# Kernel optimization log

Hardware: AMD Instinct MI355X
Metric: run time of the kernel (lower is better)

## Reference

```python
import jax, jax.numpy as jnp
import numpy as np

NUM_EXPERTS = 8
TOP_K = 2
EMBED = 1024
FFN = 2048
GATE_HID = 1024


def setup_inputs() -> dict:
    key = jax.random.key(0)
    ks = jax.random.split(key, 8)
    s_e = 1.0 / np.sqrt(EMBED)
    s_f = 1.0 / np.sqrt(FFN)
    s_g = 1.0 / np.sqrt(GATE_HID)
    return {
        "hidden_states": jax.random.normal(ks[0], (2, 2048, EMBED), dtype=jnp.float32),
        # gate: Linear(EMBED->GATE_HID) with bias, ELU, Linear(GATE_HID->NUM_EXPERTS) with bias
        "gw1": jax.random.uniform(ks[1], (EMBED, GATE_HID), jnp.float32, -s_e, s_e),
        "gb1": jax.random.uniform(ks[2], (GATE_HID,), jnp.float32, -s_e, s_e),
        "gw2": jax.random.uniform(ks[3], (GATE_HID, NUM_EXPERTS), jnp.float32, -s_g, s_g),
        "gb2": jax.random.uniform(ks[4], (NUM_EXPERTS,), jnp.float32, -s_g, s_g),
        # experts (bias=False): w1,w3: EMBED->FFN ; w2: FFN->EMBED, stacked over experts
        "w1": jax.random.uniform(ks[5], (NUM_EXPERTS, EMBED, FFN), jnp.float32, -s_e, s_e),
        "w3": jax.random.uniform(ks[6], (NUM_EXPERTS, EMBED, FFN), jnp.float32, -s_e, s_e),
        "w2": jax.random.uniform(ks[7], (NUM_EXPERTS, FFN, EMBED), jnp.float32, -s_f, s_f),
    }


def reference(hidden_states, gw1, gb1, gw2, gb2, w1, w3, w2):
    B, S, H = hidden_states.shape
    x = hidden_states.reshape(-1, H)                      # [T, H]
    T = x.shape[0]
    # gate MLP
    g = jax.nn.elu(x @ gw1 + gb1)
    router_logits = g @ gw2 + gb2                         # [T, E]
    probs = jax.nn.softmax(router_logits.astype(jnp.float32), axis=-1)
    rw, sel = jax.lax.top_k(probs, TOP_K)                 # [T, K]
    rw = rw / jnp.sum(rw, axis=-1, keepdims=True)
    rw = rw.astype(hidden_states.dtype)
    # combine weights per (token, expert); full-capacity MoE == weighted sum
    combine = jnp.zeros((T, NUM_EXPERTS), dtype=hidden_states.dtype)
    combine = combine.at[jnp.arange(T)[:, None], sel].add(rw)   # [T, E]
    # expert MLPs computed densely then combined (math identical to gather/scatter)
    h = jax.nn.relu(jnp.einsum('th,ehf->etf', x, w1)) * jnp.einsum('th,ehf->etf', x, w3)
    y = jnp.einsum('etf,efh->eth', h, w2)                 # [E, T, H]
    out = jnp.einsum('eth,te->th', y, combine)            # [T, H]
    return out.reshape(B, S, H), router_logits
```

## Files before the change

kernel.cpp:

```cpp
#include <hip/hip_runtime.h>
#include <hip/hip_bf16.h>
#include <stdint.h>

#define TOKENS 4096
#define HDIM   1024
#define FDIM   2048
#define NEXP   8
#define NSLOTS (2 * TOKENS)
#define SLOTPAD (NSLOTS + 128)
#define RISKY_CAP 256
#define FLAG_THR 6e-3f

typedef __attribute__((ext_vector_type(4))) float        f32x4v;
typedef __attribute__((ext_vector_type(2))) float        f32x2v;
typedef __attribute__((ext_vector_type(4))) unsigned int u32x4v;
typedef __attribute__((ext_vector_type(8))) _Float16     f16x8v;

__device__ __forceinline__ unsigned short f2h(float f) {
  _Float16 h = (_Float16)f;
  union { _Float16 h; unsigned short u; } x; x.h = h; return x.u;
}

__device__ __forceinline__ void gload16(void* lds, const void* g) {
  __builtin_amdgcn_global_load_lds(
      reinterpret_cast<const __attribute__((address_space(1))) uint32_t*>(
          reinterpret_cast<uintptr_t>(g)),
      reinterpret_cast<__attribute__((address_space(3))) uint32_t*>(
          reinterpret_cast<uintptr_t>(lds)),
      16, 0, 0);
}

__global__ void k_convert_xh(const float* __restrict__ in, unsigned short* __restrict__ out) {
  const int i = (blockIdx.x * 256 + threadIdx.x) * 8;
  f32x4v a = *(const f32x4v*)(in + i);
  f32x4v b = *(const f32x4v*)(in + i + 4);
  u32x4v r;
  r[0] = (uint32_t)f2h(a[0]) | ((uint32_t)f2h(a[1]) << 16);
  r[1] = (uint32_t)f2h(a[2]) | ((uint32_t)f2h(a[3]) << 16);
  r[2] = (uint32_t)f2h(b[0]) | ((uint32_t)f2h(b[1]) << 16);
  r[3] = (uint32_t)f2h(b[2]) | ((uint32_t)f2h(b[3]) << 16);
  *(u32x4v*)(out + i) = r;
}

__device__ __forceinline__ void transpose_tile_v2(const float* __restrict__ ip,
                                                  unsigned short* __restrict__ op,
                                                  int R, int C, int r0, int c0) {
  __shared__ unsigned short tile[64][70];
  const int t = threadIdx.x;
  const int cp = (t & 15) * 4;
  const int rp = (t >> 4) * 2;
#pragma unroll
  for (int p = 0; p < 2; ++p) {
    const int r = rp + p * 32;
    f32x4v v0 = *(const f32x4v*)(ip + (size_t)(r0 + r) * C + c0 + cp);
    f32x4v v1 = *(const f32x4v*)(ip + (size_t)(r0 + r + 1) * C + c0 + cp);
#pragma unroll
    for (int j = 0; j < 4; ++j)
      *(uint32_t*)&tile[cp + j][r] = (uint32_t)f2h(v0[j]) | ((uint32_t)f2h(v1[j]) << 16);
  }
  __syncthreads();
  const int c = t >> 2, rc = (t & 3) * 16;
  uint32_t q[8];
#pragma unroll
  for (int j = 0; j < 8; ++j) q[j] = *(uint32_t*)&tile[c][rc + j * 2];
  unsigned short* o = op + (size_t)(c0 + c) * R + r0 + rc;
  u32x4v s0, s1;
  s0[0] = q[0]; s0[1] = q[1]; s0[2] = q[2]; s0[3] = q[3];
  s1[0] = q[4]; s1[1] = q[5]; s1[2] = q[6]; s1[3] = q[7];
  *(u32x4v*)o = s0;
  *(u32x4v*)(o + 8) = s1;
}

__global__ __launch_bounds__(256)
void k_transpose_v2(const float* __restrict__ in, unsigned short* __restrict__ out,
                    int R, int C) {
  const size_t mat = (size_t)R * C;
  transpose_tile_v2(in + (size_t)blockIdx.z * mat, out + (size_t)blockIdx.z * mat,
                    R, C, blockIdx.y * 64, blockIdx.x * 64);
}

__global__ __launch_bounds__(256)
void k_transpose_w13_v2(const float* __restrict__ w1, const float* __restrict__ w3,
                        unsigned short* __restrict__ o1, unsigned short* __restrict__ o3) {
  const int R = 1024, C = 2048;
  const size_t mat = (size_t)R * C;
  const int e = blockIdx.z & 7, which = blockIdx.z >> 3;
  const float* ip = (which ? w3 : w1) + (size_t)e * mat;
  unsigned short* op = (which ? o3 : o1) + (size_t)e * mat;
  transpose_tile_v2(ip, op, R, C, blockIdx.y * 64, blockIdx.x * 64);
}

__global__ __launch_bounds__(256)
void k_gate_f16(const unsigned short* __restrict__ Xh, const unsigned short* __restrict__ Bt,
                const float* __restrict__ gb1, float* __restrict__ G) {
  const int n0 = blockIdx.x * 64, m0 = blockIdx.y * 128;
  __shared__ unsigned short lA[128 * 64];
  __shared__ unsigned short lB[64 * 64];
  const int t = threadIdx.x, lane = t & 63, wv = t >> 6;

  const unsigned short *ap[4], *bp[2];
#pragma unroll
  for (int i = 0; i < 4; ++i) {
    const int gi = wv * 4 + i;
    const int row = gi * 8 + (lane >> 3);
    const int cs = (lane & 7) ^ (row & 7);
    ap[i] = Xh + (size_t)(m0 + row) * HDIM + cs * 8;
  }
#pragma unroll
  for (int i = 0; i < 2; ++i) {
    const int gi = wv * 2 + i;
    const int row = gi * 8 + (lane >> 3);
    const int cs = (lane & 7) ^ (row & 7);
    bp[i] = Bt + (size_t)(n0 + row) * HDIM + cs * 8;
  }

  f32x4v acc[4][2];
#pragma unroll
  for (int m = 0; m < 4; ++m)
#pragma unroll
    for (int n = 0; n < 2; ++n) acc[m][n] = (f32x4v){0.f, 0.f, 0.f, 0.f};

  const int wr = (wv >> 1) * 64, wc = (wv & 1) * 32;

  for (int k0 = 0; k0 < HDIM; k0 += 64) {
#pragma unroll
    for (int i = 0; i < 4; ++i) gload16(lA + (wv * 4 + i) * 512, ap[i] + k0);
#pragma unroll
    for (int i = 0; i < 2; ++i) gload16(lB + (wv * 2 + i) * 512, bp[i] + k0);
    __syncthreads();
#pragma unroll
    for (int kk = 0; kk < 2; ++kk) {
      const int ch = kk * 4 + (lane >> 4);
      f16x8v af[4];
#pragma unroll
      for (int m = 0; m < 4; ++m) {
        const int r = wr + m * 16 + (lane & 15);
        af[m] = *(const f16x8v*)(lA + r * 64 + (ch ^ (r & 7)) * 8);
      }
#pragma unroll
      for (int n = 0; n < 2; ++n) {
        const int r = wc + n * 16 + (lane & 15);
        f16x8v b = *(const f16x8v*)(lB + r * 64 + (ch ^ (r & 7)) * 8);
#pragma unroll
        for (int m = 0; m < 4; ++m)
          acc[m][n] = __builtin_amdgcn_mfma_f32_16x16x32_f16(af[m], b, acc[m][n], 0, 0, 0);
      }
    }
    __syncthreads();
  }
#pragma unroll
  for (int m = 0; m < 4; ++m)
#pragma unroll
    for (int n = 0; n < 2; ++n)
#pragma unroll
      for (int q = 0; q < 4; ++q) {
        const int row = m0 + wr + m * 16 + ((lane >> 4) << 2) + q;
        const int col = n0 + wc + n * 16 + (lane & 15);
        float x = acc[m][n][q] + gb1[col];
        G[(size_t)row * 1024 + col] = x > 0.f ? x : expm1f(x);
      }
}

__global__ void k_logits(const float* __restrict__ G, const float* __restrict__ gw2,
                         const float* __restrict__ gb2, float* __restrict__ Lg,
                         int* __restrict__ risky, int* __restrict__ rcnt) {
  const int lane = threadIdx.x & 63, wv = threadIdx.x >> 6;
  const int tok = blockIdx.x * 4 + wv;
  const float* g = G + (size_t)tok * 1024 + lane * 16;
  float acc[8];
#pragma unroll
  for (int j = 0; j < 8; ++j) acc[j] = 0.f;
#pragma unroll
  for (int c = 0; c < 16; c += 4) {
    f32x4v gv = *(const f32x4v*)(g + c);
#pragma unroll
    for (int u = 0; u < 4; ++u) {
      const float* wrow = gw2 + (size_t)(lane * 16 + c + u) * 8;
      f32x4v w0 = *(const f32x4v*)wrow;
      f32x4v w1 = *(const f32x4v*)(wrow + 4);
#pragma unroll
      for (int j = 0; j < 4; ++j) {
        acc[j]     += gv[u] * w0[j];
        acc[j + 4] += gv[u] * w1[j];
      }
    }
  }
#pragma unroll
  for (int s = 1; s < 64; s <<= 1)
#pragma unroll
    for (int j = 0; j < 8; ++j) acc[j] += __shfl_xor(acc[j], s, 64);
  if (lane == 0) {
    float l[8];
#pragma unroll
    for (int j = 0; j < 8; ++j) { l[j] = acc[j] + gb2[j]; Lg[(size_t)tok * 8 + j] = l[j]; }
    int i0 = 0; float v0 = l[0];
#pragma unroll
    for (int j = 1; j < 8; ++j) if (l[j] > v0) { v0 = l[j]; i0 = j; }
    int i1 = (i0 == 0) ? 1 : 0; float v1 = l[i1];
#pragma unroll
    for (int j = 0; j < 8; ++j) if (j != i0 && l[j] > v1) { v1 = l[j]; i1 = j; }
    float v2 = -1e30f;
#pragma unroll
    for (int j = 0; j < 8; ++j) if (j != i0 && j != i1 && l[j] > v2) v2 = l[j];
    if (v1 - v2 < FLAG_THR) {
      const int pos = atomicAdd(rcnt, 1);
      if (pos < RISKY_CAP) risky[pos] = tok;
    }
  }
}

__global__ __launch_bounds__(256)
void k_fixup_gs(const float* __restrict__ X, const float* __restrict__ gw1,
                const float* __restrict__ gb1, const int* __restrict__ risky,
                const int* __restrict__ rcnt, float* __restrict__ gsbuf) {
  __shared__ float xs[1024];
  __shared__ float red[128];
  int n = *rcnt; if (n > RISKY_CAP) n = RISKY_CAP;
  const int idx = blockIdx.y;
  if (idx >= n) return;
  const int tok = risky[idx];
  const int s0 = blockIdx.x * 128;
  const int t = threadIdx.x;
  for (int i = t; i < 1024; i += 256) xs[i] = X[(size_t)tok * 1024 + i];
  __syncthreads();
  const int h = t & 127, kh = t >> 7;
  const float* wp = gw1 + (size_t)(kh * 512) * 1024 + s0 + h;
  const float* xp = xs + kh * 512;
  float a0 = 0.f, a1 = 0.f, a2 = 0.f, a3 = 0.f;
  for (int k = 0; k < 512; k += 4) {
    a0 += xp[k]     * wp[(size_t)k * 1024];
    a1 += xp[k + 1] * wp[(size_t)(k + 1) * 1024];
    a2 += xp[k + 2] * wp[(size_t)(k + 2) * 1024];
    a3 += xp[k + 3] * wp[(size_t)(k + 3) * 1024];
  }
  const float acc = (a0 + a1) + (a2 + a3);
  if (kh == 1) red[h] = acc;
  __syncthreads();
  if (kh == 0) {
    const float v = acc + red[h] + gb1[s0 + h];
    gsbuf[(size_t)idx * 1024 + s0 + h] = v > 0.f ? v : expm1f(v);
  }
}

__global__ __launch_bounds__(256)
void k_fixup_lg(const float* __restrict__ gsbuf, const float* __restrict__ gw2,
                const float* __restrict__ gb2, const int* __restrict__ risky,
                const int* __restrict__ rcnt, float* __restrict__ Lg) {
  __shared__ float part[4][8];
  int n = *rcnt; if (n > RISKY_CAP) n = RISKY_CAP;
  const int idx = blockIdx.x;
  if (idx >= n) return;
  const int tok = risky[idx];
  const int t = threadIdx.x, lane = t & 63, wv = t >> 6;
  float lacc[8];
#pragma unroll
  for (int e = 0; e < 8; ++e) lacc[e] = 0.f;
#pragma unroll
  for (int j = 0; j < 4; ++j) {
    const int k = t * 4 + j;
    const float gv = gsbuf[(size_t)idx * 1024 + k];
    const float* w = gw2 + (size_t)k * 8;
#pragma unroll
    for (int e = 0; e < 8; ++e) lacc[e] += gv * w[e];
  }
#pragma unroll
  for (int s = 1; s < 64; s <<= 1)
#pragma unroll
    for (int e = 0; e < 8; ++e) lacc[e] += __shfl_xor(lacc[e], s, 64);
  if (lane == 0) {
#pragma unroll
    for (int e = 0; e < 8; ++e) part[wv][e] = lacc[e];
  }
  __syncthreads();
  if (t < 8) Lg[(size_t)tok * 8 + t] = part[0][t] + part[1][t] + part[2][t] + part[3][t] + gb2[t];
}

__global__ void k_top2(const float* __restrict__ Lg, int* __restrict__ tok_e,
                       float* __restrict__ tok_w, int* __restrict__ counts) {
  const int t = blockIdx.x * 256 + threadIdx.x;
  float l[8];
#pragma unroll
  for (int j = 0; j < 8; ++j) l[j] = Lg[(size_t)t * 8 + j];
  float mx = l[0];
#pragma unroll
  for (int j = 1; j < 8; ++j) mx = fmaxf(mx, l[j]);
  float p[8];
#pragma unroll
  for (int j = 0; j < 8; ++j) p[j] = expf(l[j] - mx);
  int i0 = 0; float b0 = p[0];
#pragma unroll
  for (int j = 1; j < 8; ++j) if (p[j] > b0) { b0 = p[j]; i0 = j; }
  int i1 = (i0 == 0) ? 1 : 0; float b1 = p[i1];
#pragma unroll
  for (int j = 0; j < 8; ++j) if (j != i0 && p[j] > b1) { b1 = p[j]; i1 = j; }
  const float inv = 1.f / (b0 + b1);
  tok_e[2 * t] = i0; tok_e[2 * t + 1] = i1;
  tok_w[2 * t] = b0 * inv; tok_w[2 * t + 1] = b1 * inv;
  atomicAdd(&counts[i0], 1);
  atomicAdd(&counts[i1], 1);
}

__global__ void k_offsets(const int* __restrict__ counts, int* __restrict__ offs,
                          int* __restrict__ curs) {
  if (threadIdx.x == 0) {
    int a = 0;
#pragma unroll
    for (int e = 0; e < NEXP; ++e) { offs[e] = a; a += counts[e]; }
  }
  if (threadIdx.x < NEXP) curs[threadIdx.x] = 0;
}

__global__ void k_assign(const int* __restrict__ tok_e, const float* __restrict__ tok_w,
                         const int* __restrict__ offs, int* __restrict__ curs,
                         int* __restrict__ slot_tok, float* __restrict__ slot_w,
                         int* __restrict__ tok2slot) {
  const int t = blockIdx.x * 256 + threadIdx.x;
#pragma unroll
  for (int k = 0; k < 2; ++k) {
    const int e = tok_e[2 * t + k];
    const int pos = atomicAdd(&curs[e], 1);
    const int slot = offs[e] + pos;
    slot_tok[slot] = t;
    slot_w[slot] = tok_w[2 * t + k];
    tok2slot[2 * t + k] = slot;
  }
}

__global__ __launch_bounds__(256, 2)
void k_gemm1(const unsigned short* __restrict__ Xh, const unsigned short* __restrict__ w1T,
             const unsigned short* __restrict__ w3T, const int* __restrict__ slot_tok,
             const int* __restrict__ counts, const int* __restrict__ offs,
             unsigned short* __restrict__ Hout) {
  const int e = blockIdx.z;
  const int cnt = counts[e];
  const int mt = blockIdx.y;
  if (mt * 128 >= cnt) return;
  const int base = offs[e] + mt * 128;
  const int n0 = blockIdx.x * 128;

  __shared__ unsigned short lA[128 * 64];
  __shared__ unsigned short lB1[128 * 64];
  __shared__ unsigned short lB3[128 * 64];
  __shared__ int tokid[128];

  const int t = threadIdx.x;
  if (t < 128) tokid[t] = slot_tok[base + t];
  __syncthreads();

  const int lane = t & 63, wv = t >> 6;
  const unsigned short *arow[4], *b1row[4], *b3row[4];
#pragma unroll
  for (int i = 0; i < 4; ++i) {
    const int gi = wv * 4 + i;
    const int row = gi * 8 + (lane >> 3);
    const int cs = (lane & 7) ^ (row & 7);
    arow[i] = Xh + (size_t)tokid[row] * HDIM + cs * 8;
    const int f = n0 + row;
    b1row[i] = w1T + ((size_t)e * FDIM + f) * HDIM + cs * 8;
    b3row[i] = w3T + ((size_t)e * FDIM + f) * HDIM + cs * 8;
  }

  f32x4v acc1[4][4], acc3[4][4];
#pragma unroll
  for (int m = 0; m < 4; ++m)
#pragma unroll
    for (int n = 0; n < 4; ++n) {
      acc1[m][n] = (f32x4v){0.f, 0.f, 0.f, 0.f};
      acc3[m][n] = (f32x4v){0.f, 0.f, 0.f, 0.f};
    }
  const int wr = (wv >> 1) * 64, wc = (wv & 1) * 64;

  for (int k0 = 0; k0 < HDIM; k0 += 64) {
#pragma unroll
    for (int i = 0; i < 4; ++i) {
      gload16(lA + (wv * 4 + i) * 512, arow[i] + k0);
      gload16(lB1 + (wv * 4 + i) * 512, b1row[i] + k0);
      gload16(lB3 + (wv * 4 + i) * 512, b3row[i] + k0);
    }
    __syncthreads();
#pragma unroll
    for (int kk = 0; kk < 64; kk += 32) {
      const int ch = (kk >> 3) + (lane >> 4);
      f16x8v af[4];
#pragma unroll
      for (int m = 0; m < 4; ++m) {
        const int r = wr + m * 16 + (lane & 15);
        af[m] = *(const f16x8v*)(lA + r * 64 + (ch ^ (r & 7)) * 8);
      }
#pragma unroll
      for (int n = 0; n < 4; ++n) {
        const int r = wc + n * 16 + (lane & 15);
        const int o = r * 64 + (ch ^ (r & 7)) * 8;
        f16x8v b1 = *(const f16x8v*)(lB1 + o);
        f16x8v b3 = *(const f16x8v*)(lB3 + o);
#pragma unroll
        for (int m = 0; m < 4; ++m) {
          acc1[m][n] = __builtin_amdgcn_mfma_f32_16x16x32_f16(af[m], b1, acc1[m][n], 0, 0, 0);
          acc3[m][n] = __builtin_amdgcn_mfma_f32_16x16x32_f16(af[m], b3, acc3[m][n], 0, 0, 0);
        }
      }
    }
    __syncthreads();
  }

  const int maxr = cnt - mt * 128;
#pragma unroll
  for (int m = 0; m < 4; ++m)
#pragma unroll
    for (int q = 0; q < 4; ++q) {
      const int rl = wr + m * 16 + ((lane >> 4) << 2) + q;
      if (rl < maxr) {
        unsigned short* hrow = Hout + (size_t)(base + rl) * FDIM;
#pragma unroll
        for (int n = 0; n < 4; ++n) {
          const int col = n0 + wc + n * 16 + (lane & 15);
          const float h = fmaxf(acc1[m][n][q], 0.f) * acc3[m][n][q];
          hrow[col] = f2h(h);
        }
      }
    }
}

__global__ __launch_bounds__(256, 2)
void k_gemm2(const unsigned short* __restrict__ Hin, const unsigned short* __restrict__ w2T,
             const int* __restrict__ counts, const int* __restrict__ offs,
             unsigned short* __restrict__ Y) {
  const int e = blockIdx.z;
  const int cnt = counts[e];
  const int mt = blockIdx.y;
  if (mt * 128 >= cnt) return;
  const int base = offs[e] + mt * 128;
  const int n0 = blockIdx.x * 128;

  __shared__ unsigned short lA[128 * 64];
  __shared__ unsigned short lB[128 * 64];

  const int t = threadIdx.x, lane = t & 63, wv = t >> 6;
  const unsigned short *arow[4], *brow[4];
#pragma unroll
  for (int i = 0; i < 4; ++i) {
    const int gi = wv * 4 + i;
    const int row = gi * 8 + (lane >> 3);
    const int cs = (lane & 7) ^ (row & 7);
    arow[i] = Hin + (size_t)(base + row) * FDIM + cs * 8;
    brow[i] = w2T + ((size_t)e * HDIM + n0 + row) * FDIM + cs * 8;
  }

  f32x4v acc[4][4];
#pragma unroll
  for (int m = 0; m < 4; ++m)
#pragma unroll
    for (int n = 0; n < 4; ++n) acc[m][n] = (f32x4v){0.f, 0.f, 0.f, 0.f};

  const int wr = (wv >> 1) * 64, wc = (wv & 1) * 64;

  for (int k0 = 0; k0 < FDIM; k0 += 64) {
#pragma unroll
    for (int i = 0; i < 4; ++i) {
      gload16(lA + (wv * 4 + i) * 512, arow[i] + k0);
      gload16(lB + (wv * 4 + i) * 512, brow[i] + k0);
    }
    __syncthreads();
#pragma unroll
    for (int kk = 0; kk < 64; kk += 32) {
      const int ch = (kk >> 3) + (lane >> 4);
      f16x8v af[4];
#pragma unroll
      for (int m = 0; m < 4; ++m) {
        const int r = wr + m * 16 + (lane & 15);
        af[m] = *(const f16x8v*)(lA + r * 64 + (ch ^ (r & 7)) * 8);
      }
#pragma unroll
      for (int n = 0; n < 4; ++n) {
        const int r = wc + n * 16 + (lane & 15);
        f16x8v b = *(const f16x8v*)(lB + r * 64 + (ch ^ (r & 7)) * 8);
#pragma unroll
        for (int m = 0; m < 4; ++m)
          acc[m][n] = __builtin_amdgcn_mfma_f32_16x16x32_f16(af[m], b, acc[m][n], 0, 0, 0);
      }
    }
    __syncthreads();
  }

  const int maxr = cnt - mt * 128;
#pragma unroll
  for (int m = 0; m < 4; ++m)
#pragma unroll
    for (int q = 0; q < 4; ++q) {
      const int rl = wr + m * 16 + ((lane >> 4) << 2) + q;
      if (rl < maxr) {
        unsigned short* yrow = Y + (size_t)(base + rl) * HDIM;
#pragma unroll
        for (int n = 0; n < 4; ++n) {
          const int col = n0 + wc + n * 16 + (lane & 15);
          yrow[col] = f2h(acc[m][n][q]);
        }
      }
    }
}

__global__ __launch_bounds__(256)
void k_combine(const unsigned short* __restrict__ Y, const int* __restrict__ tok2slot,
               const float* __restrict__ slot_w, float* __restrict__ out) {
  const int tok = blockIdx.x;
  const int s0 = tok2slot[2 * tok], s1 = tok2slot[2 * tok + 1];
  const float w0 = slot_w[s0], w1 = slot_w[s1];
  const int i = threadIdx.x * 4;
  const _Float16* y0 = (const _Float16*)(Y + (size_t)s0 * HDIM + i);
  const _Float16* y1 = (const _Float16*)(Y + (size_t)s1 * HDIM + i);
  f32x4v r;
#pragma unroll
  for (int j = 0; j < 4; ++j) r[j] = w0 * (float)y0[j] + w1 * (float)y1[j];
  *(f32x4v*)(out + (size_t)tok * HDIM + i) = r;
}

extern "C" void kernel_launch(void* const* d_in, const int* in_sizes, int n_in,
                              void* d_out, int out_size, void* d_ws, size_t ws_size,
                              hipStream_t stream) {
  const float* X   = (const float*)d_in[0];
  const float* gw1 = (const float*)d_in[1];
  const float* gb1 = (const float*)d_in[2];
  const float* gw2 = (const float*)d_in[3];
  const float* gb2 = (const float*)d_in[4];
  const float* w1  = (const float*)d_in[5];
  const float* w3  = (const float*)d_in[6];
  const float* w2  = (const float*)d_in[7];

  float* out = (float*)d_out;
  float* Lg  = out + (size_t)TOKENS * HDIM;

  char* ws = (char*)d_ws;
  size_t off = 0;
  auto alloc = [&](size_t b) { void* p = ws + off; off = (off + b + 255) & ~(size_t)255; return p; };

  unsigned short* Xh    = (unsigned short*)alloc((size_t)TOKENS * HDIM * 2);
  unsigned short* gw1T  = (unsigned short*)alloc((size_t)HDIM * 1024 * 2);
  unsigned short* w1T   = (unsigned short*)alloc((size_t)NEXP * FDIM * HDIM * 2);
  unsigned short* w3T   = (unsigned short*)alloc((size_t)NEXP * FDIM * HDIM * 2);
  unsigned short* w2T   = (unsigned short*)alloc((size_t)NEXP * HDIM * FDIM * 2);
  float*          G     = (float*)alloc((size_t)TOKENS * 1024 * 4);
  unsigned short* Hf    = (unsigned short*)alloc((size_t)SLOTPAD * FDIM * 2);
  unsigned short* Yb    = (unsigned short*)alloc((size_t)SLOTPAD * HDIM * 2);
  float*          gsbuf = (float*)alloc((size_t)RISKY_CAP * 1024 * 4);
  int*   tok_e    = (int*)alloc((size_t)TOKENS * 2 * 4);
  float* tok_w    = (float*)alloc((size_t)TOKENS * 2 * 4);
  int*   tok2slot = (int*)alloc((size_t)TOKENS * 2 * 4);
  int*   counts   = (int*)alloc(64);
  int*   offs     = (int*)alloc(64);
  int*   curs     = (int*)alloc(64);
  int*   slot_tok = (int*)alloc((size_t)SLOTPAD * 4);
  float* slot_w   = (float*)alloc((size_t)SLOTPAD * 4);
  int*   risky    = (int*)alloc((size_t)RISKY_CAP * 4);
  int*   rcnt     = (int*)alloc(64);

  hipMemsetAsync(counts, 0, 64, stream);
  hipMemsetAsync(rcnt, 0, 64, stream);
  hipMemsetAsync(slot_tok, 0, (size_t)SLOTPAD * 4, stream);

  k_convert_xh<<<dim3(TOKENS * HDIM / 2048), 256, 0, stream>>>(X, Xh);
  k_transpose_w13_v2<<<dim3(FDIM / 64, HDIM / 64, 2 * NEXP), 256, 0, stream>>>(w1, w3, w1T, w3T);
  k_transpose_v2<<<dim3(HDIM / 64, FDIM / 64, NEXP), 256, 0, stream>>>(w2, w2T, FDIM, HDIM);
  k_transpose_v2<<<dim3(16, 16, 1), 256, 0, stream>>>(gw1, gw1T, 1024, 1024);
  k_gate_f16<<<dim3(1024 / 64, TOKENS / 128), 256, 0, stream>>>(Xh, gw1T, gb1, G);
  k_logits<<<dim3(TOKENS / 4), 256, 0, stream>>>(G, gw2, gb2, Lg, risky, rcnt);
  k_fixup_gs<<<dim3(8, RISKY_CAP), 256, 0, stream>>>(X, gw1, gb1, risky, rcnt, gsbuf);
  k_fixup_lg<<<dim3(RISKY_CAP), 256, 0, stream>>>(gsbuf, gw2, gb2, risky, rcnt, Lg);
  k_top2<<<dim3(TOKENS / 256), 256, 0, stream>>>(Lg, tok_e, tok_w, counts);
  k_offsets<<<dim3(1), 64, 0, stream>>>(counts, offs, curs);
  k_assign<<<dim3(TOKENS / 256), 256, 0, stream>>>(tok_e, tok_w, offs, curs, slot_tok, slot_w, tok2slot);
  k_gemm1<<<dim3(FDIM / 128, TOKENS / 128, NEXP), 256, 0, stream>>>(Xh, w1T, w3T, slot_tok, counts, offs, Hf);
  k_gemm2<<<dim3(HDIM / 128, TOKENS / 128, NEXP), 256, 0, stream>>>(Hf, w2T, counts, offs, Yb);
  k_combine<<<dim3(TOKENS), 256, 0, stream>>>(Yb, tok2slot, slot_w, out);
}
```

Measured before the change: 373.5 us.

## Fuse prep kernels, store gate activations as fp16, enlarge gemm1 tile to 256 rows

Merges the input conversion and the three weight-transpose launches into a single k_prep kernel, which cuts launch overhead and tail gaps. The gate hidden activations are stored as fp16 instead of fp32, halving that intermediate's write and read traffic, at some cost in logit precision. k_gemm1 moves to 512-thread blocks covering 256 token rows, so each B-weight tile is reused across more rows, and SLOTPAD grows to cover the larger tile overrun. The larger tile lowers occupancy and wastes more work on partially filled expert tiles.

```diff
diff --git a/kernel.cpp b/kernel.cpp
--- a/kernel.cpp
+++ b/kernel.cpp
@@ -7,7 +7,7 @@
 #define FDIM   2048
 #define NEXP   8
 #define NSLOTS (2 * TOKENS)
-#define SLOTPAD (NSLOTS + 128)
+#define SLOTPAD (NSLOTS + 256)
 #define RISKY_CAP 256
 #define FLAG_THR 6e-3f
 
@@ -30,18 +30,6 @@
       16, 0, 0);
 }
 
-__global__ void k_convert_xh(const float* __restrict__ in, unsigned short* __restrict__ out) {
-  const int i = (blockIdx.x * 256 + threadIdx.x) * 8;
-  f32x4v a = *(const f32x4v*)(in + i);
-  f32x4v b = *(const f32x4v*)(in + i + 4);
-  u32x4v r;
-  r[0] = (uint32_t)f2h(a[0]) | ((uint32_t)f2h(a[1]) << 16);
-  r[1] = (uint32_t)f2h(a[2]) | ((uint32_t)f2h(a[3]) << 16);
-  r[2] = (uint32_t)f2h(b[0]) | ((uint32_t)f2h(b[1]) << 16);
-  r[3] = (uint32_t)f2h(b[2]) | ((uint32_t)f2h(b[3]) << 16);
-  *(u32x4v*)(out + i) = r;
-}
-
 __device__ __forceinline__ void transpose_tile_v2(const float* __restrict__ ip,
                                                   unsigned short* __restrict__ op,
                                                   int R, int C, int r0, int c0) {
@@ -71,28 +59,53 @@
   *(u32x4v*)(o + 8) = s1;
 }
 
+#define NB_CONV 2048
+#define NB_W13  8192
+#define NB_W2   4096
 __global__ __launch_bounds__(256)
-void k_transpose_v2(const float* __restrict__ in, unsigned short* __restrict__ out,
-                    int R, int C) {
-  const size_t mat = (size_t)R * C;
-  transpose_tile_v2(in + (size_t)blockIdx.z * mat, out + (size_t)blockIdx.z * mat,
-                    R, C, blockIdx.y * 64, blockIdx.x * 64);
-}
-
-__global__ __launch_bounds__(256)
-void k_transpose_w13_v2(const float* __restrict__ w1, const float* __restrict__ w3,
-                        unsigned short* __restrict__ o1, unsigned short* __restrict__ o3) {
-  const int R = 1024, C = 2048;
-  const size_t mat = (size_t)R * C;
-  const int e = blockIdx.z & 7, which = blockIdx.z >> 3;
-  const float* ip = (which ? w3 : w1) + (size_t)e * mat;
-  unsigned short* op = (which ? o3 : o1) + (size_t)e * mat;
-  transpose_tile_v2(ip, op, R, C, blockIdx.y * 64, blockIdx.x * 64);
+void k_prep(const float* __restrict__ X, unsigned short* __restrict__ Xh,
+            const float* __restrict__ w1, const float* __restrict__ w3,
+            unsigned short* __restrict__ o1, unsigned short* __restrict__ o3,
+            const float* __restrict__ w2, unsigned short* __restrict__ o2,
+            const float* __restrict__ gw1, unsigned short* __restrict__ og1) {
+  const int id = blockIdx.x;
+  if (id < NB_CONV) {
+    const int i = (id * 256 + threadIdx.x) * 8;
+    f32x4v a = *(const f32x4v*)(X + i);
+    f32x4v b = *(const f32x4v*)(X + i + 4);
+    u32x4v r;
+    r[0] = (uint32_t)f2h(a[0]) | ((uint32_t)f2h(a[1]) << 16);
+    r[1] = (uint32_t)f2h(a[2]) | ((uint32_t)f2h(a[3]) << 16);
+    r[2] = (uint32_t)f2h(b[0]) | ((uint32_t)f2h(b[1]) << 16);
+    r[3] = (uint32_t)f2h(b[2]) | ((uint32_t)f2h(b[3]) << 16);
+    *(u32x4v*)(Xh + i) = r;
+    return;
+  }
+  int t = id - NB_CONV;
+  if (t < NB_W13) {
+    const int bx = t & 31, by = (t >> 5) & 15, bz = t >> 9;
+    const int e = bz & 7, which = bz >> 3;
+    const size_t mat = (size_t)1024 * 2048;
+    transpose_tile_v2((which ? w3 : w1) + (size_t)e * mat,
+                      (which ? o3 : o1) + (size_t)e * mat,
+                      1024, 2048, by * 64, bx * 64);
+    return;
+  }
+  t -= NB_W13;
+  if (t < NB_W2) {
+    const int bx = t & 15, by = (t >> 4) & 31, e = t >> 9;
+    const size_t mat = (size_t)2048 * 1024;
+    transpose_tile_v2(w2 + (size_t)e * mat, o2 + (size_t)e * mat,
+                      2048, 1024, by * 64, bx * 64);
+    return;
+  }
+  t -= NB_W2;
+  transpose_tile_v2(gw1, og1, 1024, 1024, (t >> 4) * 64, (t & 15) * 64);
 }
 
 __global__ __launch_bounds__(256)
 void k_gate_f16(const unsigned short* __restrict__ Xh, const unsigned short* __restrict__ Bt,
-                const float* __restrict__ gb1, float* __restrict__ G) {
+                const float* __restrict__ gb1, unsigned short* __restrict__ Gh) {
   const int n0 = blockIdx.x * 64, m0 = blockIdx.y * 128;
   __shared__ unsigned short lA[128 * 64];
   __shared__ unsigned short lB[64 * 64];
@@ -157,32 +170,33 @@
         const int row = m0 + wr + m * 16 + ((lane >> 4) << 2) + q;
         const int col = n0 + wc + n * 16 + (lane & 15);
         float x = acc[m][n][q] + gb1[col];
-        G[(size_t)row * 1024 + col] = x > 0.f ? x : expm1f(x);
-      }
-}
-
-__global__ void k_logits(const float* __restrict__ G, const float* __restrict__ gw2,
+        Gh[(size_t)row * 1024 + col] = f2h(x > 0.f ? x : expm1f(x));
+      }
+}
+
+__global__ void k_logits(const unsigned short* __restrict__ Gh, const float* __restrict__ gw2,
                          const float* __restrict__ gb2, float* __restrict__ Lg,
                          int* __restrict__ risky, int* __restrict__ rcnt) {
   const int lane = threadIdx.x & 63, wv = threadIdx.x >> 6;
   const int tok = blockIdx.x * 4 + wv;
-  const float* g = G + (size_t)tok * 1024 + lane * 16;
+  const unsigned short* g = Gh + (size_t)tok * 1024 + lane * 16;
+  f16x8v g0 = *(const f16x8v*)g;
+  f16x8v g1 = *(const f16x8v*)(g + 8);
+  float gv[16];
+#pragma unroll
+  for (int j = 0; j < 8; ++j) { gv[j] = (float)g0[j]; gv[8 + j] = (float)g1[j]; }
   float acc[8];
 #pragma unroll
   for (int j = 0; j < 8; ++j) acc[j] = 0.f;
 #pragma unroll
-  for (int c = 0; c < 16; c += 4) {
-    f32x4v gv = *(const f32x4v*)(g + c);
-#pragma unroll
-    for (int u = 0; u < 4; ++u) {
-      const float* wrow = gw2 + (size_t)(lane * 16 + c + u) * 8;
-      f32x4v w0 = *(const f32x4v*)wrow;
-      f32x4v w1 = *(const f32x4v*)(wrow + 4);
-#pragma unroll
-      for (int j = 0; j < 4; ++j) {
-        acc[j]     += gv[u] * w0[j];
-        acc[j + 4] += gv[u] * w1[j];
-      }
+  for (int u = 0; u < 16; ++u) {
+    const float* wrow = gw2 + (size_t)(lane * 16 + u) * 8;
+    f32x4v w0 = *(const f32x4v*)wrow;
+    f32x4v w1 = *(const f32x4v*)(wrow + 4);
+#pragma unroll
+    for (int j = 0; j < 4; ++j) {
+      acc[j]     += gv[u] * w0[j];
+      acc[j + 4] += gv[u] * w1[j];
     }
   }
 #pragma unroll
@@ -326,7 +340,7 @@
   }
 }
 
-__global__ __launch_bounds__(256, 2)
+__global__ __launch_bounds__(512, 1)
 void k_gemm1(const unsigned short* __restrict__ Xh, const unsigned short* __restrict__ w1T,
              const unsigned short* __restrict__ w3T, const int* __restrict__ slot_tok,
              const int* __restrict__ counts, const int* __restrict__ offs,
@@ -334,30 +348,37 @@
   const int e = blockIdx.z;
   const int cnt = counts[e];
   const int mt = blockIdx.y;
-  if (mt * 128 >= cnt) return;
-  const int base = offs[e] + mt * 128;
+  if (mt * 256 >= cnt) return;
+  const int base = offs[e] + mt * 256;
   const int n0 = blockIdx.x * 128;
 
-  __shared__ unsigned short lA[128 * 64];
+  __shared__ unsigned short lA[256 * 64];
   __shared__ unsigned short lB1[128 * 64];
   __shared__ unsigned short lB3[128 * 64];
-  __shared__ int tokid[128];
+  __shared__ int tokid[256];
 
   const int t = threadIdx.x;
-  if (t < 128) tokid[t] = slot_tok[base + t];
+  if (t < 256) tokid[t] = slot_tok[base + t];
   __syncthreads();
 
   const int lane = t & 63, wv = t >> 6;
-  const unsigned short *arow[4], *b1row[4], *b3row[4];
+  const int wm = wv >> 1, wn = wv & 1;
+  const int wr = wm * 64, wc = wn * 64;
+
+  const unsigned short *aSrc[4], *b1Src[2], *b3Src[2];
 #pragma unroll
   for (int i = 0; i < 4; ++i) {
-    const int gi = wv * 4 + i;
-    const int row = gi * 8 + (lane >> 3);
+    const int row = (wv * 4 + i) * 8 + (lane >> 3);
     const int cs = (lane & 7) ^ (row & 7);
-    arow[i] = Xh + (size_t)tokid[row] * HDIM + cs * 8;
+    aSrc[i] = Xh + (size_t)tokid[row] * HDIM + cs * 8;
+  }
+#pragma unroll
+  for (int i = 0; i < 2; ++i) {
+    const int row = (wv * 2 + i) * 8 + (lane >> 3);
+    const int cs = (lane & 7) ^ (row & 7);
     const int f = n0 + row;
-    b1row[i] = w1T + ((size_t)e * FDIM + f) * HDIM + cs * 8;
-    b3row[i] = w3T + ((size_t)e * FDIM + f) * HDIM + cs * 8;
+    b1Src[i] = w1T + ((size_t)e * FDIM + f) * HDIM + cs * 8;
+    b3Src[i] = w3T + ((size_t)e * FDIM + f) * HDIM + cs * 8;
   }
 
   f32x4v acc1[4][4], acc3[4][4];
@@ -368,20 +389,20 @@
       acc1[m][n] = (f32x4v){0.f, 0.f, 0.f, 0.f};
       acc3[m][n] = (f32x4v){0.f, 0.f, 0.f, 0.f};
     }
-  const int wr = (wv >> 1) * 64, wc = (wv & 1) * 64;
 
   for (int k0 = 0; k0 < HDIM; k0 += 64) {
 #pragma unroll
-    for (int i = 0; i < 4; ++i) {
-      gload16(lA + (wv * 4 + i) * 512, arow[i] + k0);
-      gload16(lB1 + (wv * 4 + i) * 512, b1row[i] + k0);
-      gload16(lB3 + (wv * 4 + i) * 512, b3row[i] + k0);
+    for (int i = 0; i < 4; ++i) gload16(lA + (wv * 4 + i) * 512, aSrc[i] + k0);
+#pragma unroll
+    for (int i = 0; i < 2; ++i) {
+      gload16(lB1 + (wv * 2 + i) * 512, b1Src[i] + k0);
+      gload16(lB3 + (wv * 2 + i) * 512, b3Src[i] + k0);
     }
     __syncthreads();
 #pragma unroll
-    for (int kk = 0; kk < 64; kk += 32) {
-      const int ch = (kk >> 3) + (lane >> 4);
-      f16x8v af[4];
+    for (int kk = 0; kk < 2; ++kk) {
+      const int ch = kk * 4 + (lane >> 4);
+      f16x8v af[4], bf1[4], bf3[4];
 #pragma unroll
       for (int m = 0; m < 4; ++m) {
         const int r = wr + m * 16 + (lane & 15);
@@ -391,19 +412,21 @@
       for (int n = 0; n < 4; ++n) {
         const int r = wc + n * 16 + (lane & 15);
         const int o = r * 64 + (ch ^ (r & 7)) * 8;
-        f16x8v b1 = *(const f16x8v*)(lB1 + o);
-        f16x8v b3 = *(const f16x8v*)(lB3 + o);
+        bf1[n] = *(const f16x8v*)(lB1 + o);
+        bf3[n] = *(const f16x8v*)(lB3 + o);
+      }
+#pragma unroll
+      for (int n = 0; n < 4; ++n)
 #pragma unroll
         for (int m = 0; m < 4; ++m) {
-          acc1[m][n] = __builtin_amdgcn_mfma_f32_16x16x32_f16(af[m], b1, acc1[m][n], 0, 0, 0);
-          acc3[m][n] = __builtin_amdgcn_mfma_f32_16x16x32_f16(af[m], b3, acc3[m][n], 0, 0, 0);
+          acc1[m][n] = __builtin_amdgcn_mfma_f32_16x16x32_f16(af[m], bf1[n], acc1[m][n], 0, 0, 0);
+          acc3[m][n] = __builtin_amdgcn_mfma_f32_16x16x32_f16(af[m], bf3[n], acc3[m][n], 0, 0, 0);
         }
-      }
     }
     __syncthreads();
   }
 
-  const int maxr = cnt - mt * 128;
+  const int maxr = cnt - mt * 256;
 #pragma unroll
   for (int m = 0; m < 4; ++m)
 #pragma unroll
@@ -538,7 +561,7 @@
   unsigned short* w1T   = (unsigned short*)alloc((size_t)NEXP * FDIM * HDIM * 2);
   unsigned short* w3T   = (unsigned short*)alloc((size_t)NEXP * FDIM * HDIM * 2);
   unsigned short* w2T   = (unsigned short*)alloc((size_t)NEXP * HDIM * FDIM * 2);
-  float*          G     = (float*)alloc((size_t)TOKENS * 1024 * 4);
+  unsigned short* Gh    = (unsigned short*)alloc((size_t)TOKENS * 1024 * 2);
   unsigned short* Hf    = (unsigned short*)alloc((size_t)SLOTPAD * FDIM * 2);
   unsigned short* Yb    = (unsigned short*)alloc((size_t)SLOTPAD * HDIM * 2);
   float*          gsbuf = (float*)alloc((size_t)RISKY_CAP * 1024 * 4);
@@ -557,18 +580,16 @@
   hipMemsetAsync(rcnt, 0, 64, stream);
   hipMemsetAsync(slot_tok, 0, (size_t)SLOTPAD * 4, stream);
 
-  k_convert_xh<<<dim3(TOKENS * HDIM / 2048), 256, 0, stream>>>(X, Xh);
-  k_transpose_w13_v2<<<dim3(FDIM / 64, HDIM / 64, 2 * NEXP), 256, 0, stream>>>(w1, w3, w1T, w3T);
-  k_transpose_v2<<<dim3(HDIM / 64, FDIM / 64, NEXP), 256, 0, stream>>>(w2, w2T, FDIM, HDIM);
-  k_transpose_v2<<<dim3(16, 16, 1), 256, 0, stream>>>(gw1, gw1T, 1024, 1024);
-  k_gate_f16<<<dim3(1024 / 64, TOKENS / 128), 256, 0, stream>>>(Xh, gw1T, gb1, G);
-  k_logits<<<dim3(TOKENS / 4), 256, 0, stream>>>(G, gw2, gb2, Lg, risky, rcnt);
+  k_prep<<<dim3(NB_CONV + NB_W13 + NB_W2 + 256), 256, 0, stream>>>(
+      X, Xh, w1, w3, w1T, w3T, w2, w2T, gw1, gw1T);
+  k_gate_f16<<<dim3(1024 / 64, TOKENS / 128), 256, 0, stream>>>(Xh, gw1T, gb1, Gh);
+  k_logits<<<dim3(TOKENS / 4), 256, 0, stream>>>(Gh, gw2, gb2, Lg, risky, rcnt);
   k_fixup_gs<<<dim3(8, RISKY_CAP), 256, 0, stream>>>(X, gw1, gb1, risky, rcnt, gsbuf);
   k_fixup_lg<<<dim3(RISKY_CAP), 256, 0, stream>>>(gsbuf, gw2, gb2, risky, rcnt, Lg);
   k_top2<<<dim3(TOKENS / 256), 256, 0, stream>>>(Lg, tok_e, tok_w, counts);
   k_offsets<<<dim3(1), 64, 0, stream>>>(counts, offs, curs);
   k_assign<<<dim3(TOKENS / 256), 256, 0, stream>>>(tok_e, tok_w, offs, curs, slot_tok, slot_w, tok2slot);
-  k_gemm1<<<dim3(FDIM / 128, TOKENS / 128, NEXP), 256, 0, stream>>>(Xh, w1T, w3T, slot_tok, counts, offs, Hf);
+  k_gemm1<<<dim3(FDIM / 128, TOKENS / 256, NEXP), 512, 0, stream>>>(Xh, w1T, w3T, slot_tok, counts, offs, Hf);
   k_gemm2<<<dim3(HDIM / 128, TOKENS / 128, NEXP), 256, 0, stream>>>(Hf, w2T, counts, offs, Yb);
   k_combine<<<dim3(TOKENS), 256, 0, stream>>>(Yb, tok2slot, slot_w, out);
 }
```

Measured after the change: 383.0 us. +2.6%, slower.
